# Optimization experiments

Measured on AMD Instinct MI355X. Metric: run time of the kernel, lower is better.

The kernel has to match this reference:

```python
import jax, jax.numpy as jnp
import numpy as np

B, S, D, H, KV, HD = 2, 1024, 4096, 32, 8, 128
GROUP = H // KV


def setup_inputs() -> dict:
    key = jax.random.key(0)
    ks = jax.random.split(key, 9)
    x = jax.random.normal(ks[0], (B, S, D), dtype=jnp.float32)
    # RoPE tables: [max_seq_len, head_dim] (half-duplicated frequencies)
    pos = jnp.arange(S, dtype=jnp.float32)
    inv_freq = 1.0 / (10000.0 ** (jnp.arange(0, HD, 2, dtype=jnp.float32) / HD))
    freqs = pos[:, None] * inv_freq[None, :]            # [S, HD/2]
    emb = jnp.concatenate([freqs, freqs], axis=-1)      # [S, HD]
    cos, sin = jnp.cos(emb), jnp.sin(emb)
    # causal mask: True = masked
    mask = jnp.triu(jnp.ones((S, S), dtype=bool), 1)[None, None]  # [1,1,S,S]
    def qw(k, o, i):
        return jax.random.randint(k, (o, i), -127, 128, dtype=jnp.int8)
    wq = qw(ks[1], H * HD, D)
    wk = qw(ks[2], KV * HD, D)
    wv = qw(ks[3], KV * HD, D)
    wo = qw(ks[4], D, H * HD)
    sq = jnp.float32(0.02); sk = jnp.float32(0.02)
    sv = jnp.float32(0.02); so = jnp.float32(0.02)
    bq = jax.random.normal(ks[5], (H * HD,), jnp.float32) * 0.01
    bk = jax.random.normal(ks[6], (KV * HD,), jnp.float32) * 0.01
    bv = jax.random.normal(ks[7], (KV * HD,), jnp.float32) * 0.01
    return dict(x=x, mask=mask, cos=cos, sin=sin,
                wq=wq, bq=bq, sq=sq, wk=wk, bk=bk, sk=sk,
                wv=wv, bv=bv, sv=sv, wo=wo, so=so, start_pos=0)


def _deq_linear(x, w_int8, scale, bias):
    # dequantize-on-the-fly int8 linear: y = x @ (w.astype * scale).T + b
    w = w_int8.astype(x.dtype) * scale                  # [O, I]
    y = jnp.einsum('bsi,oi->bso', x, w)
    return y if bias is None else y + bias


def _rope(x, cos, sin, offset):
    # x: [b, s, h, hd]
    hd = x.shape[-1]
    x1, x2 = x[..., : hd // 2], x[..., hd // 2 :]
    s_len = x.shape[1]
    c = cos[offset : offset + s_len][None, :, None, :]
    s = sin[offset : offset + s_len][None, :, None, :]
    rotated = jnp.concatenate([-x2, x1], axis=-1)
    return (x * c + rotated * s).astype(x.dtype)


def reference(x, mask, cos, sin, wq, bq, sq, wk, bk, sk, wv, bv, sv, wo, so, start_pos):
    b, seq, _ = x.shape
    xq = _deq_linear(x, wq, sq, bq).reshape(b, seq, H, HD)
    xk = _deq_linear(x, wk, sk, bk).reshape(b, seq, KV, HD)
    xv = _deq_linear(x, wv, sv, bv).reshape(b, seq, KV, HD)
    xq = _rope(xq, cos, sin, start_pos)
    xk = _rope(xk, cos, sin, start_pos)
    # KV cache: start_pos=0 prefill -> cache[:start_pos+seq] == (xk, xv)
    kv_idx = jnp.arange(H) // GROUP                      # q head -> kv head
    keys = xk[:, :, kv_idx, :]                           # [b, kv_len, H, hd]
    values = xv[:, :, kv_idx, :]
    scores = jnp.einsum('bqhd,bkhd->bhqk', xq, keys) / np.sqrt(HD).astype(np.float32)
    scores = jnp.where(mask, -jnp.inf, scores)
    probs = jax.nn.softmax(scores, axis=-1)
    out = jnp.einsum('bhqk,bkhd->bqhd', probs, values).reshape(b, seq, H * HD)
    return _deq_linear(out, wo, so, None)
```

## Files before the change

kernel.cpp:

```cpp
#include <hip/hip_runtime.h>
#include <hip/hip_bf16.h>
#include <hip/hip_fp16.h>
#include <cstdint>

typedef _Float16 f16;
typedef _Float16 f16x8 __attribute__((ext_vector_type(8)));
typedef _Float16 f16x4 __attribute__((ext_vector_type(4)));
typedef float f32x4 __attribute__((ext_vector_type(4)));

#define DEV_INLINE __device__ __forceinline__

DEV_INLINE void async_ld16(const void* g, void* l) {
  __builtin_amdgcn_global_load_lds((const __attribute__((address_space(1))) void*)g,
                                   (__attribute__((address_space(3))) void*)l, 16, 0, 0);
}

template <int N>
DEV_INLINE void wait_vm() {
  static_assert(N >= 0 && N <= 12, "gate range");
  if constexpr (N == 0)  asm volatile("s_waitcnt vmcnt(0)" ::: "memory");
  if constexpr (N == 1)  asm volatile("s_waitcnt vmcnt(1)" ::: "memory");
  if constexpr (N == 2)  asm volatile("s_waitcnt vmcnt(2)" ::: "memory");
  if constexpr (N == 3)  asm volatile("s_waitcnt vmcnt(3)" ::: "memory");
  if constexpr (N == 4)  asm volatile("s_waitcnt vmcnt(4)" ::: "memory");
  if constexpr (N == 5)  asm volatile("s_waitcnt vmcnt(5)" ::: "memory");
  if constexpr (N == 6)  asm volatile("s_waitcnt vmcnt(6)" ::: "memory");
  if constexpr (N == 7)  asm volatile("s_waitcnt vmcnt(7)" ::: "memory");
  if constexpr (N == 8)  asm volatile("s_waitcnt vmcnt(8)" ::: "memory");
  if constexpr (N == 9)  asm volatile("s_waitcnt vmcnt(9)" ::: "memory");
  if constexpr (N == 10) asm volatile("s_waitcnt vmcnt(10)" ::: "memory");
  if constexpr (N == 11) asm volatile("s_waitcnt vmcnt(11)" ::: "memory");
  if constexpr (N == 12) asm volatile("s_waitcnt vmcnt(12)" ::: "memory");
}
DEV_INLINE void lgk0() {
  asm volatile("s_waitcnt lgkmcnt(0)" ::: "memory");
  __builtin_amdgcn_sched_barrier(0);
}


__global__ __launch_bounds__(256) void k_cast_x_split(const float* __restrict__ x,
                                                      f16* __restrict__ acat) {
  int idx = blockIdx.x * 256 + threadIdx.x;
  int i = idx * 4;
  if (i >= 2048 * 4096) return;
  float4 v = *(const float4*)&x[i];
  int row = i >> 12, col = i & 4095;
  f16 h0 = (f16)v.x, h1 = (f16)v.y, h2 = (f16)v.z, h3 = (f16)v.w;
  f16x4 hi = {h0, h1, h2, h3};
  f16x4 lo = {(f16)(v.x - (float)h0), (f16)(v.y - (float)h1),
              (f16)(v.z - (float)h2), (f16)(v.w - (float)h3)};
  size_t base = (size_t)row * 8192 + col;
  *(f16x4*)&acat[base] = hi;
  *(f16x4*)&acat[base + 4096] = lo;
}

__global__ __launch_bounds__(256) void k_cast_i32_f16(const int* __restrict__ w,
                                                      f16* __restrict__ out, int n) {
  int i = (blockIdx.x * 256 + threadIdx.x) * 4;
  if (i >= n) return;
  int4 v = *(const int4*)&w[i];
  f16x4 o = {(f16)(float)v.x, (f16)(float)v.y, (f16)(float)v.z, (f16)(float)v.w};
  *(f16x4*)&out[i] = o;
}

__global__ __launch_bounds__(256) void k_prep_w(
    const int* __restrict__ wq, const int* __restrict__ wk, const int* __restrict__ wv,
    const float* __restrict__ bq, const float* __restrict__ bk, const float* __restrict__ bv,
    const float* __restrict__ sq, const float* __restrict__ sk, const float* __restrict__ sv,
    f16* __restrict__ wcat, float* __restrict__ bias_cat, float* __restrict__ scale_cat) {
  int i = blockIdx.x * 256 + threadIdx.x;
  if (i < 6291456) {
    int e = i * 4, row = e >> 12, col = e & 4095;
    int4 v;
    if (row < 4096)      v = *(const int4*)&wq[(size_t)row * 4096 + col];
    else if (row < 5120) v = *(const int4*)&wk[(size_t)(row - 4096) * 4096 + col];
    else                 v = *(const int4*)&wv[(size_t)(row - 5120) * 4096 + col];
    f16x4 o = {(f16)(float)v.x, (f16)(float)v.y, (f16)(float)v.z, (f16)(float)v.w};
    *(f16x4*)&wcat[e] = o;
  }
  if (i < 6144) {
    float b, s;
    if (i < 4096)      { b = bq[i];        s = sq[0]; }
    else if (i < 5120) { b = bk[i - 4096]; s = sk[0]; }
    else               { b = bv[i - 5120]; s = sv[0]; }
    bias_cat[i] = b;
    scale_cat[i] = s;
  }
}

template <int BM, int BN, int MODE>
__global__ __launch_bounds__(512) void k_gemm6(
    const f16* __restrict__ A, const f16* __restrict__ W,
    f16* __restrict__ o_hi, f16* __restrict__ o_lo, float* __restrict__ o_f32,
    const float* __restrict__ scale_vec, const float* __restrict__ bias_vec,
    const float* __restrict__ scale_scalar,
    int N, int K, int kmask, int ldw, int nym) {
  constexpr int WM = 2, WN = 4;
  constexpr int MR = BM / WM / 16;
  constexpr int NR = BN / WN / 16;
  constexpr int NH = NR / 2;
  constexpr int AKC = BM * 64;
  constexpr int BKC = BN * 64;
  constexpr int SLOT = 2 * (AKC + BKC);
  constexpr int LAH = AKC / 8192;
  constexpr int LBH = BKC / 8192;
  constexpr int GS = 2 * LBH + 3;
  constexpr int GT1 = 2 * LBH + 2;
  constexpr int GT2 = LBH + 1;
  extern __shared__ __align__(16) char lds[];

  const int t = threadIdx.x, w = t >> 6, ln = t & 63;
  const int lr = ln & 15, lg = ln >> 4;
  const int wn = w & 3, wm = w >> 2;

  const int nwg = gridDim.x;
  const int q8 = nwg >> 3, r8 = nwg & 7;
  const int xcd = blockIdx.x & 7, bidx = blockIdx.x >> 3;
  const int sid = (xcd < r8 ? xcd * (q8 + 1) : r8 * (q8 + 1) + (xcd - r8) * q8) + bidx;
  const int m0 = (sid % nym) * BM;
  const int n0 = (sid / nym) * BN;

  const f16* aSrc[LAH];
  const f16* bSrc[LBH];
#pragma unroll
  for (int l = 0; l < LAH; l++) {
    int ci = l * 512 + t, row = ci >> 2, c = ci & 3;
    aSrc[l] = A + (size_t)(m0 + row) * K + (c ^ ((row >> 1) & 3)) * 8;
  }
#pragma unroll
  for (int l = 0; l < LBH; l++) {
    int ci = l * 512 + t, row = ci >> 2, c = ci & 3;
    bSrc[l] = W + (size_t)(n0 + row) * ldw + (c ^ ((row >> 1) & 3)) * 8;
  }

  f32x4 acc[MR][NR] = {};
  f16x8 af[MR], bflo[NH], bfhi[NH];

  auto stageA = [&](int tt, int kc) {
    char* dst = lds + (tt & 1) * SLOT + kc * AKC;
    const int ko = tt * 64 + kc * 32;
#pragma unroll
    for (int l = 0; l < LAH; l++)
      async_ld16(aSrc[l] + ko, dst + (l * 512 + w * 64) * 16);
  };
  auto stageB = [&](int tt, int kc) {
    char* dst = lds + (tt & 1) * SLOT + 2 * AKC + kc * BKC;
    const int ko = ((tt * 64) & kmask) + kc * 32;
#pragma unroll
    for (int l = 0; l < LBH; l++)
      async_ld16(bSrc[l] + ko, dst + (l * 512 + w * 64) * 16);
  };
  auto readA = [&](int tt, int kc) {
    const char* base = lds + (tt & 1) * SLOT + kc * AKC;
#pragma unroll
    for (int mf = 0; mf < MR; mf++) {
      const int row = wm * (BM / WM) + mf * 16 + lr;
      af[mf] = *(const f16x8*)(base + row * 64 + (lg ^ ((row >> 1) & 3)) * 16);
    }
  };
  auto readB = [&](f16x8 (&dst)[NH], int tt, int nq, int kc) {
    const char* base = lds + (tt & 1) * SLOT + 2 * AKC + kc * BKC;
#pragma unroll
    for (int nf = 0; nf < NH; nf++) {
      const int row = wn * (BN / WN) + (nq * NH + nf) * 16 + lr;
      dst[nf] = *(const f16x8*)(base + row * 64 + (lg ^ ((row >> 1) & 3)) * 16);
    }
  };
  auto mma = [&](f16x8 (&b)[NH], int nq) {
    __builtin_amdgcn_s_setprio(1);
#pragma unroll
    for (int m = 0; m < MR; m++)
#pragma unroll
      for (int n = 0; n < NH; n++)
        acc[m][nq * NH + n] =
            __builtin_amdgcn_mfma_f32_16x16x32_f16(af[m], b[n], acc[m][nq * NH + n], 0, 0, 0);
    __builtin_amdgcn_s_setprio(0);
  };
  auto bar = [&]() { __builtin_amdgcn_s_barrier(); };

  const int NT = K >> 6;
  stageA(0, 0); stageB(0, 0); stageA(0, 1); stageB(0, 1);
  stageA(1, 0); stageB(1, 0); stageA(1, 1);
  wait_vm<GS>();
  bar();

  for (int tt = 0; tt + 2 < NT; ++tt) {
    stageB(tt + 1, 1);
    readA(tt, 0); readB(bflo, tt, 0, 0);
    bar(); lgk0(); mma(bflo, 0); bar();
    stageA(tt + 2, 0);
    readB(bfhi, tt, 1, 0);
    wait_vm<GS>();
    bar(); lgk0(); mma(bfhi, 1); bar();
    stageB(tt + 2, 0);
    readA(tt, 1); readB(bflo, tt, 0, 1);
    bar(); lgk0(); mma(bflo, 0); bar();
    stageA(tt + 2, 1);
    readB(bfhi, tt, 1, 1);
    wait_vm<GS>();
    bar(); lgk0(); mma(bfhi, 1); bar();
  }
  {
    const int tt = NT - 2;
    stageB(tt + 1, 1);
    readA(tt, 0); readB(bflo, tt, 0, 0);
    bar(); lgk0(); mma(bflo, 0); bar();
    readB(bfhi, tt, 1, 0);
    wait_vm<GT1>();
    bar(); lgk0(); mma(bfhi, 1); bar();
    readA(tt, 1); readB(bflo, tt, 0, 1);
    bar(); lgk0(); mma(bflo, 0); bar();
    readB(bfhi, tt, 1, 1);
    wait_vm<GT2>();
    bar(); lgk0(); mma(bfhi, 1); bar();
  }
  {
    const int tt = NT - 1;
    readA(tt, 0); readB(bflo, tt, 0, 0);
    bar(); lgk0(); mma(bflo, 0); bar();
    readB(bfhi, tt, 1, 0);
    wait_vm<0>();
    bar(); lgk0(); mma(bfhi, 1); bar();
    readA(tt, 1); readB(bflo, tt, 0, 1);
    bar(); lgk0(); mma(bflo, 0); bar();
    readB(bfhi, tt, 1, 1);
    bar(); lgk0(); mma(bfhi, 1);
  }

#pragma unroll
  for (int n = 0; n < NR; n++) {
    const int col = n0 + wn * (BN / WN) + n * 16 + lr;
    const float sc = (MODE == 0) ? scale_vec[col] : scale_scalar[0];
    const float bs = (MODE == 0) ? bias_vec[col] : 0.f;
#pragma unroll
    for (int m = 0; m < MR; m++)
#pragma unroll
      for (int r2 = 0; r2 < 4; r2++) {
        const int row = m0 + wm * (BM / WM) + m * 16 + lg * 4 + r2;
        const float v = acc[m][n][r2] * sc + bs;
        if constexpr (MODE == 0) {
          f16 h = (f16)v;
          o_hi[(size_t)row * N + col] = h;
          o_lo[(size_t)row * N + col] = (f16)(v - (float)h);
        } else {
          o_f32[(size_t)row * N + col] = v;
        }
      }
  }
}

__global__ __launch_bounds__(256) void k_rope(f16* __restrict__ XH, f16* __restrict__ XL,
                                              const float* __restrict__ cosT,
                                              const float* __restrict__ sinT,
                                              const int* __restrict__ sp) {
  int idx = blockIdx.x * 256 + threadIdx.x;
  if (idx >= 2048 * 40 * 64) return;
  int p = idx & 63;
  int hh = (idx >> 6) % 40;
  int tkn = idx / (40 * 64);
  int col = (hh < 32) ? hh * 128 + p : 4096 + (hh - 32) * 128 + p;
  size_t i1 = (size_t)tkn * 6144 + col, i2 = i1 + 64;
  float x1 = (float)XH[i1] + (float)XL[i1];
  float x2 = (float)XH[i2] + (float)XL[i2];
  int pos = (tkn & 1023) + sp[0];
  float c = cosT[pos * 128 + p], s = sinT[pos * 128 + p];
  float o1 = x1 * c - x2 * s;
  float o2 = x2 * c + x1 * s;
  f16 h1 = (f16)o1, h2 = (f16)o2;
  XH[i1] = h1; XL[i1] = (f16)(o1 - (float)h1);
  XH[i2] = h2; XL[i2] = (f16)(o2 - (float)h2);
}

__global__ __launch_bounds__(512) void k_attn3(const f16* __restrict__ XH,
                                               const f16* __restrict__ XL,
                                               f16* __restrict__ out) {
  __shared__ __align__(16) f16 KsH[32 * 152];
  __shared__ __align__(16) f16 KsL[32 * 152];
  __shared__ __align__(16) f16 VT[128 * 40];
  __shared__ __align__(16) f16 Pb[8 * 16 * 40];
  const int t = threadIdx.x, w = t >> 6, l = t & 63;
  const int lr = l & 15, lg = l >> 4;
  const int id = blockIdx.x;
  const int kvh = id & 7;
  const int j = id >> 3;
  const int qb = j & 7;
  const int hg = (j >> 3) & 3;
  const int b = j >> 5;
  const int h = kvh * 4 + hg;
  const int q0 = qb * 128;
  const size_t rs_ = 6144;
  const f16* Qh = XH + ((size_t)(b * 1024 + q0)) * rs_ + h * 128;
  const f16* Ql_ = XL + ((size_t)(b * 1024 + q0)) * rs_ + h * 128;
  const f16* KhG = XH + ((size_t)(b * 1024)) * rs_ + 4096 + kvh * 128;
  const f16* KlG = XL + ((size_t)(b * 1024)) * rs_ + 4096 + kvh * 128;
  const f16* VG = XH + ((size_t)(b * 1024)) * rs_ + 5120 + kvh * 128;

  f16x8 qh[4], ql[4];
  {
    size_t qoff = (size_t)(w * 16 + lr) * rs_ + lg * 8;
#pragma unroll
    for (int c = 0; c < 4; c++) {
      qh[c] = *(const f16x8*)(Qh + qoff + c * 32);
      ql[c] = *(const f16x8*)(Ql_ + qoff + c * 32);
    }
  }
  f32x4 accd[8] = {};
  float m_r[4], l_r[4];
#pragma unroll
  for (int r = 0; r < 4; r++) { m_r[r] = -1e30f; l_r[r] = 0.f; }

  const int nkv = q0 + 128;
  for (int kv0 = 0; kv0 < nkv; kv0 += 32) {
    __syncthreads();
    {
      int row = t >> 4, ch = t & 15;
      size_t go = (size_t)(kv0 + row) * rs_ + ch * 8;
      *(f16x8*)&KsH[row * 152 + ch * 8] = *(const f16x8*)(KhG + go);
      *(f16x8*)&KsL[row * 152 + ch * 8] = *(const f16x8*)(KlG + go);
    }
    {
      int row = t & 31, d8 = t >> 5;
      f16x8 vv = *(const f16x8*)(VG + (size_t)(kv0 + row) * rs_ + d8 * 8);
#pragma unroll
      for (int jj = 0; jj < 8; jj++) VT[(d8 * 8 + jj) * 40 + row] = vv[jj];
    }
    __syncthreads();

    f32x4 sc[2] = {};
#pragma unroll
    for (int cb = 0; cb < 2; cb++)
#pragma unroll
      for (int c = 0; c < 4; c++) {
        const f16x8 kh = *(const f16x8*)&KsH[(cb * 16 + lr) * 152 + c * 32 + lg * 8];
        const f16x8 kl = *(const f16x8*)&KsL[(cb * 16 + lr) * 152 + c * 32 + lg * 8];
        sc[cb] = __builtin_amdgcn_mfma_f32_16x16x32_f16(qh[c], kh, sc[cb], 0, 0, 0);
        sc[cb] = __builtin_amdgcn_mfma_f32_16x16x32_f16(qh[c], kl, sc[cb], 0, 0, 0);
        sc[cb] = __builtin_amdgcn_mfma_f32_16x16x32_f16(ql[c], kh, sc[cb], 0, 0, 0);
      }

    const float scale = 0.088388347648318447f;
    float alpha[4], pv[2][4];
#pragma unroll
    for (int r = 0; r < 4; r++) {
      const int qg = q0 + w * 16 + lg * 4 + r;
      float mx = -1e30f;
#pragma unroll
      for (int cb = 0; cb < 2; cb++) {
        const int kg = kv0 + cb * 16 + lr;
        float s = sc[cb][r] * scale;
        s = (kg <= qg) ? s : -1e30f;
        pv[cb][r] = s;
        mx = fmaxf(mx, s);
      }
      mx = fmaxf(mx, __shfl_xor(mx, 1));
      mx = fmaxf(mx, __shfl_xor(mx, 2));
      mx = fmaxf(mx, __shfl_xor(mx, 4));
      mx = fmaxf(mx, __shfl_xor(mx, 8));
      const float mn = fmaxf(m_r[r], mx);
      alpha[r] = __expf(m_r[r] - mn);
      m_r[r] = mn;
      float rsum = 0.f;
#pragma unroll
      for (int cb = 0; cb < 2; cb++) {
        const int kg = kv0 + cb * 16 + lr;
        const float p = (kg <= qg) ? __expf(pv[cb][r] - mn) : 0.f;
        pv[cb][r] = p;
        rsum += p;
      }
      rsum += __shfl_xor(rsum, 1);
      rsum += __shfl_xor(rsum, 2);
      rsum += __shfl_xor(rsum, 4);
      rsum += __shfl_xor(rsum, 8);
      l_r[r] = l_r[r] * alpha[r] + rsum;
    }

    f16* Pw = &Pb[w * 16 * 40];
#pragma unroll
    for (int r = 0; r < 4; r++)
#pragma unroll
      for (int cb = 0; cb < 2; cb++)
        Pw[(lg * 4 + r) * 40 + cb * 16 + lr] = (f16)pv[cb][r];
    const f16x8 pf = *(const f16x8*)&Pw[lr * 40 + lg * 8];

#pragma unroll
    for (int dc = 0; dc < 8; dc++) {
      const f16x8 vf = *(const f16x8*)&VT[(dc * 16 + lr) * 40 + lg * 8];
#pragma unroll
      for (int r = 0; r < 4; r++) accd[dc][r] *= alpha[r];
      accd[dc] = __builtin_amdgcn_mfma_f32_16x16x32_f16(pf, vf, accd[dc], 0, 0, 0);
    }
  }

#pragma unroll
  for (int dc = 0; dc < 8; dc++)
#pragma unroll
    for (int r = 0; r < 4; r++) {
      const int row = b * 1024 + q0 + w * 16 + lg * 4 + r;
      out[(size_t)row * 4096 + h * 128 + dc * 16 + lr] = (f16)(accd[dc][r] / l_r[r]);
    }
}

extern "C" void kernel_launch(void* const* d_in, const int* in_sizes, int n_in,
                              void* d_out, int out_size, void* d_ws, size_t ws_size,
                              hipStream_t stream) {
  const float* x = (const float*)d_in[0];
  const float* cosT = (const float*)d_in[2];
  const float* sinT = (const float*)d_in[3];
  const int* wq = (const int*)d_in[4];
  const float* bq = (const float*)d_in[5];
  const float* sq = (const float*)d_in[6];
  const int* wk = (const int*)d_in[7];
  const float* bk = (const float*)d_in[8];
  const float* sk = (const float*)d_in[9];
  const int* wv = (const int*)d_in[10];
  const float* bv = (const float*)d_in[11];
  const float* sv = (const float*)d_in[12];
  const int* wo = (const int*)d_in[13];
  const float* so = (const float*)d_in[14];
  const int* sp = (const int*)d_in[15];

  char* ws = (char*)d_ws;
  f16* Acat = (f16*)ws;
  f16* Wcat = (f16*)(ws + 33554432);
  f16* XH = (f16*)(ws + 83886080);
  f16* XL = (f16*)(ws + 109051904);
  f16* AO = (f16*)(ws + 134217728);
  float* biasv = (float*)(ws + 150994944);
  float* scalev = (float*)(ws + 151019520);

  hipFuncSetAttribute(reinterpret_cast<const void*>(&k_gemm6<128, 384, 0>),
                      hipFuncAttributeMaxDynamicSharedMemorySize, 131072);
  hipFuncSetAttribute(reinterpret_cast<const void*>(&k_gemm6<128, 256, 1>),
                      hipFuncAttributeMaxDynamicSharedMemorySize, 98304);

  k_cast_x_split<<<8192, 256, 0, stream>>>(x, Acat);
  k_prep_w<<<24576, 256, 0, stream>>>(wq, wk, wv, bq, bk, bv, sq, sk, sv,
                                      Wcat, biasv, scalev);

  k_gemm6<128, 384, 0><<<256, 512, 131072, stream>>>(
      Acat, Wcat, XH, XL, nullptr, scalev, biasv, nullptr, 6144, 8192, 4095, 4096, 16);

  k_rope<<<20480, 256, 0, stream>>>(XH, XL, cosT, sinT, sp);

  f16* Wo_ = Acat;
  k_cast_i32_f16<<<16384, 256, 0, stream>>>(wo, Wo_, 16777216);

  k_attn3<<<512, 512, 0, stream>>>(XH, XL, AO);

  k_gemm6<128, 256, 1><<<256, 512, 98304, stream>>>(
      AO, Wo_, nullptr, nullptr, (float*)d_out, nullptr, nullptr, so, 4096, 4096,
      0x7fffffff, 4096, 16);
}
```

Baseline: 476.9 us.

## Merge prep kernels, vectorize RoPE, and prefetch K/V tiles in attention

Combines the x split-cast and QKV weight cast into one launch so a kernel launch is saved. Rewrites RoPE so each thread handles four elements with vector loads and stores instead of scalar ones. In attention, the next K/V tile is loaded into registers while the current tile is computed, then written to LDS after a barrier, hiding global load latency at the cost of extra registers and an additional barrier per iteration.

Measured after the change: 479.9 us. Within noise of the previous version (+0.6%).

```diff
diff --git a/kernel.cpp b/kernel.cpp
--- a/kernel.cpp
+++ b/kernel.cpp
@@ -37,21 +37,45 @@
   __builtin_amdgcn_sched_barrier(0);
 }
 
-
-__global__ __launch_bounds__(256) void k_cast_x_split(const float* __restrict__ x,
-                                                      f16* __restrict__ acat) {
-  int idx = blockIdx.x * 256 + threadIdx.x;
-  int i = idx * 4;
-  if (i >= 2048 * 4096) return;
-  float4 v = *(const float4*)&x[i];
-  int row = i >> 12, col = i & 4095;
-  f16 h0 = (f16)v.x, h1 = (f16)v.y, h2 = (f16)v.z, h3 = (f16)v.w;
-  f16x4 hi = {h0, h1, h2, h3};
-  f16x4 lo = {(f16)(v.x - (float)h0), (f16)(v.y - (float)h1),
-              (f16)(v.z - (float)h2), (f16)(v.w - (float)h3)};
-  size_t base = (size_t)row * 8192 + col;
-  *(f16x4*)&acat[base] = hi;
-  *(f16x4*)&acat[base + 4096] = lo;
+__global__ __launch_bounds__(256) void k_prep_all(
+    const float* __restrict__ x,
+    const int* __restrict__ wq, const int* __restrict__ wk, const int* __restrict__ wv,
+    const float* __restrict__ bq, const float* __restrict__ bk, const float* __restrict__ bv,
+    const float* __restrict__ sq, const float* __restrict__ sk, const float* __restrict__ sv,
+    f16* __restrict__ acat, f16* __restrict__ wcat,
+    float* __restrict__ bias_cat, float* __restrict__ scale_cat) {
+  const int bid = blockIdx.x;
+  if (bid < 8192) {
+    int i = (bid * 256 + threadIdx.x) * 4;
+    float4 v = *(const float4*)&x[i];
+    int row = i >> 12, col = i & 4095;
+    f16 h0 = (f16)v.x, h1 = (f16)v.y, h2 = (f16)v.z, h3 = (f16)v.w;
+    f16x4 hi = {h0, h1, h2, h3};
+    f16x4 lo = {(f16)(v.x - (float)h0), (f16)(v.y - (float)h1),
+                (f16)(v.z - (float)h2), (f16)(v.w - (float)h3)};
+    size_t base = (size_t)row * 8192 + col;
+    *(f16x4*)&acat[base] = hi;
+    *(f16x4*)&acat[base + 4096] = lo;
+  } else {
+    int i = (bid - 8192) * 256 + threadIdx.x;
+    if (i < 6291456) {
+      int e = i * 4, row = e >> 12, col = e & 4095;
+      int4 v;
+      if (row < 4096)      v = *(const int4*)&wq[(size_t)row * 4096 + col];
+      else if (row < 5120) v = *(const int4*)&wk[(size_t)(row - 4096) * 4096 + col];
+      else                 v = *(const int4*)&wv[(size_t)(row - 5120) * 4096 + col];
+      f16x4 o = {(f16)(float)v.x, (f16)(float)v.y, (f16)(float)v.z, (f16)(float)v.w};
+      *(f16x4*)&wcat[e] = o;
+    }
+    if (i < 6144) {
+      float b, s;
+      if (i < 4096)      { b = bq[i];        s = sq[0]; }
+      else if (i < 5120) { b = bk[i - 4096]; s = sk[0]; }
+      else               { b = bv[i - 5120]; s = sv[0]; }
+      bias_cat[i] = b;
+      scale_cat[i] = s;
+    }
+  }
 }
 
 __global__ __launch_bounds__(256) void k_cast_i32_f16(const int* __restrict__ w,
@@ -61,31 +85,6 @@
   int4 v = *(const int4*)&w[i];
   f16x4 o = {(f16)(float)v.x, (f16)(float)v.y, (f16)(float)v.z, (f16)(float)v.w};
   *(f16x4*)&out[i] = o;
-}
-
-__global__ __launch_bounds__(256) void k_prep_w(
-    const int* __restrict__ wq, const int* __restrict__ wk, const int* __restrict__ wv,
-    const float* __restrict__ bq, const float* __restrict__ bk, const float* __restrict__ bv,
-    const float* __restrict__ sq, const float* __restrict__ sk, const float* __restrict__ sv,
-    f16* __restrict__ wcat, float* __restrict__ bias_cat, float* __restrict__ scale_cat) {
-  int i = blockIdx.x * 256 + threadIdx.x;
-  if (i < 6291456) {
-    int e = i * 4, row = e >> 12, col = e & 4095;
-    int4 v;
-    if (row < 4096)      v = *(const int4*)&wq[(size_t)row * 4096 + col];
-    else if (row < 5120) v = *(const int4*)&wk[(size_t)(row - 4096) * 4096 + col];
-    else                 v = *(const int4*)&wv[(size_t)(row - 5120) * 4096 + col];
-    f16x4 o = {(f16)(float)v.x, (f16)(float)v.y, (f16)(float)v.z, (f16)(float)v.w};
-    *(f16x4*)&wcat[e] = o;
-  }
-  if (i < 6144) {
-    float b, s;
-    if (i < 4096)      { b = bq[i];        s = sq[0]; }
-    else if (i < 5120) { b = bk[i - 4096]; s = sk[0]; }
-    else               { b = bv[i - 5120]; s = sv[0]; }
-    bias_cat[i] = b;
-    scale_cat[i] = s;
-  }
 }
 
 template <int BM, int BN, int MODE>
@@ -249,29 +248,40 @@
   }
 }
 
-__global__ __launch_bounds__(256) void k_rope(f16* __restrict__ XH, f16* __restrict__ XL,
-                                              const float* __restrict__ cosT,
-                                              const float* __restrict__ sinT,
-                                              const int* __restrict__ sp) {
+__global__ __launch_bounds__(256) void k_rope2(f16* __restrict__ XH, f16* __restrict__ XL,
+                                               const float* __restrict__ cosT,
+                                               const float* __restrict__ sinT,
+                                               const int* __restrict__ sp) {
   int idx = blockIdx.x * 256 + threadIdx.x;
-  if (idx >= 2048 * 40 * 64) return;
-  int p = idx & 63;
-  int hh = (idx >> 6) % 40;
-  int tkn = idx / (40 * 64);
-  int col = (hh < 32) ? hh * 128 + p : 4096 + (hh - 32) * 128 + p;
-  size_t i1 = (size_t)tkn * 6144 + col, i2 = i1 + 64;
-  float x1 = (float)XH[i1] + (float)XL[i1];
-  float x2 = (float)XH[i2] + (float)XL[i2];
+  if (idx >= 2048 * 40 * 16) return;
+  int c4 = (idx & 15) * 4;
+  int hh = (idx >> 4) % 40;
+  int tkn = idx / (40 * 16);
+  int col = (hh < 32) ? hh * 128 : 4096 + (hh - 32) * 128;
+  size_t i1 = (size_t)tkn * 6144 + col + c4, i2 = i1 + 64;
   int pos = (tkn & 1023) + sp[0];
-  float c = cosT[pos * 128 + p], s = sinT[pos * 128 + p];
-  float o1 = x1 * c - x2 * s;
-  float o2 = x2 * c + x1 * s;
-  f16 h1 = (f16)o1, h2 = (f16)o2;
-  XH[i1] = h1; XL[i1] = (f16)(o1 - (float)h1);
-  XH[i2] = h2; XL[i2] = (f16)(o2 - (float)h2);
-}
-
-__global__ __launch_bounds__(512) void k_attn3(const f16* __restrict__ XH,
+  const float4 cv = *(const float4*)&cosT[pos * 128 + c4];
+  const float4 sv = *(const float4*)&sinT[pos * 128 + c4];
+  f16x4 xh1 = *(const f16x4*)&XH[i1], xh2 = *(const f16x4*)&XH[i2];
+  f16x4 xl1 = *(const f16x4*)&XL[i1], xl2 = *(const f16x4*)&XL[i2];
+  f16x4 oh1, ol1, oh2, ol2;
+  const float cc[4] = {cv.x, cv.y, cv.z, cv.w};
+  const float ss[4] = {sv.x, sv.y, sv.z, sv.w};
+#pragma unroll
+  for (int i = 0; i < 4; i++) {
+    float x1 = (float)xh1[i] + (float)xl1[i];
+    float x2 = (float)xh2[i] + (float)xl2[i];
+    float o1 = x1 * cc[i] - x2 * ss[i];
+    float o2 = x2 * cc[i] + x1 * ss[i];
+    f16 h1 = (f16)o1, h2 = (f16)o2;
+    oh1[i] = h1; ol1[i] = (f16)(o1 - (float)h1);
+    oh2[i] = h2; ol2[i] = (f16)(o2 - (float)h2);
+  }
+  *(f16x4*)&XH[i1] = oh1; *(f16x4*)&XL[i1] = ol1;
+  *(f16x4*)&XH[i2] = oh2; *(f16x4*)&XL[i2] = ol2;
+}
+
+__global__ __launch_bounds__(512) void k_attn4(const f16* __restrict__ XH,
                                                const f16* __restrict__ XL,
                                                f16* __restrict__ out) {
   __shared__ __align__(16) f16 KsH[32 * 152];
@@ -309,22 +319,36 @@
 #pragma unroll
   for (int r = 0; r < 4; r++) { m_r[r] = -1e30f; l_r[r] = 0.f; }
 
+  const int krow_s = t >> 4, kch = t & 15;
+  const int vrow_s = t & 31, vd8 = t >> 5;
+  f16x8 khr, klr, vr;
+  auto loadKV = [&](int kv0) {
+    size_t go = (size_t)(kv0 + krow_s) * rs_ + kch * 8;
+    khr = *(const f16x8*)(KhG + go);
+    klr = *(const f16x8*)(KlG + go);
+    vr = *(const f16x8*)(VG + (size_t)(kv0 + vrow_s) * rs_ + vd8 * 8);
+  };
+  auto writeKV = [&]() {
+    *(f16x8*)&KsH[krow_s * 152 + kch * 8] = khr;
+    *(f16x8*)&KsL[krow_s * 152 + kch * 8] = klr;
+#pragma unroll
+    for (int jj = 0; jj < 8; jj++) VT[(vd8 * 8 + jj) * 40 + vrow_s] = vr[jj];
+  };
+
   const int nkv = q0 + 128;
-  for (int kv0 = 0; kv0 < nkv; kv0 += 32) {
-    __syncthreads();
-    {
-      int row = t >> 4, ch = t & 15;
-      size_t go = (size_t)(kv0 + row) * rs_ + ch * 8;
-      *(f16x8*)&KsH[row * 152 + ch * 8] = *(const f16x8*)(KhG + go);
-      *(f16x8*)&KsL[row * 152 + ch * 8] = *(const f16x8*)(KlG + go);
-    }
-    {
-      int row = t & 31, d8 = t >> 5;
-      f16x8 vv = *(const f16x8*)(VG + (size_t)(kv0 + row) * rs_ + d8 * 8);
-#pragma unroll
-      for (int jj = 0; jj < 8; jj++) VT[(d8 * 8 + jj) * 40 + row] = vv[jj];
-    }
-    __syncthreads();
+  const int NT = nkv >> 5;
+  loadKV(0);
+  wait_vm<0>();
+  writeKV();
+  __syncthreads();
+
+  for (int tt = 0; tt < NT; ++tt) {
+    const int kv0 = tt * 32;
+    const bool pf = (tt + 1 < NT);
+    if (pf) {
+      loadKV(kv0 + 32);
+      __builtin_amdgcn_sched_barrier(0);
+    }
 
     f32x4 sc[2] = {};
 #pragma unroll
@@ -380,15 +404,19 @@
 #pragma unroll
       for (int cb = 0; cb < 2; cb++)
         Pw[(lg * 4 + r) * 40 + cb * 16 + lr] = (f16)pv[cb][r];
-    const f16x8 pf = *(const f16x8*)&Pw[lr * 40 + lg * 8];
+    const f16x8 pf_ = *(const f16x8*)&Pw[lr * 40 + lg * 8];
 
 #pragma unroll
     for (int dc = 0; dc < 8; dc++) {
       const f16x8 vf = *(const f16x8*)&VT[(dc * 16 + lr) * 40 + lg * 8];
 #pragma unroll
       for (int r = 0; r < 4; r++) accd[dc][r] *= alpha[r];
-      accd[dc] = __builtin_amdgcn_mfma_f32_16x16x32_f16(pf, vf, accd[dc], 0, 0, 0);
-    }
+      accd[dc] = __builtin_amdgcn_mfma_f32_16x16x32_f16(pf_, vf, accd[dc], 0, 0, 0);
+    }
+
+    __syncthreads();
+    if (pf) writeKV();
+    __syncthreads();
   }
 
 #pragma unroll
@@ -433,19 +461,18 @@
   hipFuncSetAttribute(reinterpret_cast<const void*>(&k_gemm6<128, 256, 1>),
                       hipFuncAttributeMaxDynamicSharedMemorySize, 98304);
 
-  k_cast_x_split<<<8192, 256, 0, stream>>>(x, Acat);
-  k_prep_w<<<24576, 256, 0, stream>>>(wq, wk, wv, bq, bk, bv, sq, sk, sv,
-                                      Wcat, biasv, scalev);
+  k_prep_all<<<32768, 256, 0, stream>>>(x, wq, wk, wv, bq, bk, bv, sq, sk, sv,
+                                        Acat, Wcat, biasv, scalev);
 
   k_gemm6<128, 384, 0><<<256, 512, 131072, stream>>>(
       Acat, Wcat, XH, XL, nullptr, scalev, biasv, nullptr, 6144, 8192, 4095, 4096, 16);
 
-  k_rope<<<20480, 256, 0, stream>>>(XH, XL, cosT, sinT, sp);
+  k_rope2<<<5120, 256, 0, stream>>>(XH, XL, cosT, sinT, sp);
 
   f16* Wo_ = Acat;
   k_cast_i32_f16<<<16384, 256, 0, stream>>>(wo, Wo_, 16777216);
 
-  k_attn3<<<512, 512, 0, stream>>>(XH, XL, AO);
+  k_attn4<<<512, 512, 0, stream>>>(XH, XL, AO);
 
   k_gemm6<128, 256, 1><<<256, 512, 98304, stream>>>(
       AO, Wo_, nullptr, nullptr, (float*)d_out, nullptr, nullptr, so, 4096, 4096,
```
